# Kernel tuning notes

Measured on AMD Instinct MI355X. Metric: run time of the kernel, lower is better.

## Reference

```python
import jax, jax.numpy as jnp
import numpy as np

H = 12      # heads
P = 4       # dim_point
CHUNK = 256 # chunk_size
DIM_SINGLE = 768
DIM_PAIR = 64
B, N = 1, 1024


def setup_inputs() -> dict:
    key = jax.random.key(0)
    ks = jax.random.split(key, 24)
    s = 0.02
    d = DIM_SINGLE
    inp = {
        'single': jax.random.normal(ks[0], (B, N, d), jnp.float32),
        'pair': jax.random.normal(ks[1], (B, N, N, DIM_PAIR), jnp.float32),
        'rot': jax.random.normal(ks[2], (B, N, 3, 3), jnp.float32),
        'trans': jax.random.normal(ks[3], (B, N, 3), jnp.float32),
        # Linear weights stored as (in, out) so y = x @ W + b
        'Wq': jax.random.normal(ks[4], (d, d), jnp.float32) * s,
        'bq': jnp.zeros((d,), jnp.float32),
        'Wk': jax.random.normal(ks[5], (d, d), jnp.float32) * s,
        'bk': jnp.zeros((d,), jnp.float32),
        'Wv': jax.random.normal(ks[6], (d, d), jnp.float32) * s,
        'bv': jnp.zeros((d,), jnp.float32),
        'Wpb': jax.random.normal(ks[7], (DIM_PAIR, H), jnp.float32) * s,
        'bpb': jnp.zeros((H,), jnp.float32),
        'Wqp': jax.random.normal(ks[8], (d, H * P * 3), jnp.float32) * s,
        'bqp': jnp.zeros((H * P * 3,), jnp.float32),
        'Wkp': jax.random.normal(ks[9], (d, H * P * 3), jnp.float32) * s,
        'bkp': jnp.zeros((H * P * 3,), jnp.float32),
        'Wvp': jax.random.normal(ks[10], (d, H * P * 3), jnp.float32) * s,
        'bvp': jnp.zeros((H * P * 3,), jnp.float32),
        'Wo': jax.random.normal(ks[11], (d, d), jnp.float32) * s,
        'bo': jnp.zeros((d,), jnp.float32),
        'Wpo': jax.random.normal(ks[12], (H * P * 3, d), jnp.float32) * s,
        'bpo': jnp.zeros((d,), jnp.float32),
        'ln_g': jnp.ones((d,), jnp.float32),
        'ln_b': jnp.zeros((d,), jnp.float32),
    }
    return inp


def _layernorm(x, g, b, eps=1e-5):
    mu = jnp.mean(x, axis=-1, keepdims=True)
    var = jnp.mean((x - mu) ** 2, axis=-1, keepdims=True)
    return (x - mu) * jax.lax.rsqrt(var + eps) * g + b


def reference(single, pair, rot, trans, Wq, bq, Wk, bk, Wv, bv, Wpb, bpb,
              Wqp, bqp, Wkp, bkp, Wvp, bvp, Wo, bo, Wpo, bpo, ln_g, ln_b):
    Bs, Ns, C = single.shape
    Ch = C // H
    scale = Ch ** (-0.5)

    q = (single @ Wq + bq).reshape(Bs, Ns, H, Ch)
    k = (single @ Wk + bk).reshape(Bs, Ns, H, Ch)
    v = (single @ Wv + bv).reshape(Bs, Ns, H, Ch)

    # [B,N,N,H] -> [B,H,N,M]
    pair_bias = jnp.transpose(pair @ Wpb + bpb, (0, 3, 1, 2))

    q_pts = (single @ Wqp + bqp).reshape(Bs, Ns, H, P, 3)
    k_pts = (single @ Wkp + bkp).reshape(Bs, Ns, H, P, 3)
    v_pts = (single @ Wvp + bvp).reshape(Bs, Ns, H, P, 3)

    t = trans[:, :, None, None, :]  # [B,N,1,1,3]
    q_pts_g = jnp.einsum('bnhpd,bnde->bnhpe', q_pts, rot) + t
    k_pts_g = jnp.einsum('bnhpd,bnde->bnhpe', k_pts, rot) + t
    v_pts_g = jnp.einsum('bnhpd,bnde->bnhpe', v_pts, rot) + t

    q2_h = jnp.transpose(jnp.sum(q_pts_g ** 2, axis=(3, 4)), (0, 2, 1))  # [B,H,N]
    k2_h = jnp.transpose(jnp.sum(k_pts_g ** 2, axis=(3, 4)), (0, 2, 1))  # [B,H,N]

    scalar_logits = jnp.einsum('bnhc,bmhc->bhnm', q, k) * scale  # [B,H,N,N]

    out_scalar = jnp.zeros((Bs, Ns, H, Ch), single.dtype)
    out_points = jnp.zeros((Bs, Ns, H, P, 3), single.dtype)

    # Faithful to the original: softmax is taken PER CHUNK over the key axis,
    # and the per-chunk weighted sums are accumulated.
    for start in range(0, Ns, CHUNK):
        end = min(start + CHUNK, Ns)
        qk = jnp.einsum('bnhpd,bmhpd->bhnm', q_pts_g, k_pts_g[:, start:end])
        pt_logits = -0.5 * (q2_h[:, :, :, None] + k2_h[:, :, None, start:end]
                            - 2.0 * qk) * scale
        logits = scalar_logits[:, :, :, start:end] + pair_bias[:, :, :, start:end] + pt_logits
        attn = jax.nn.softmax(logits, axis=-1)  # [B,H,N,chunk]
        out_scalar = out_scalar + jnp.einsum('bhnm,bmhc->bnhc', attn, v[:, start:end])
        out_points = out_points + jnp.einsum('bhnm,bmhpd->bnhpd', attn, v_pts_g[:, start:end])

    weighted_scalar = out_scalar.reshape(Bs, Ns, H * Ch)
    weighted_points = out_points.reshape(Bs, Ns, H * P * 3)
    point_proj = weighted_points @ Wpo + bpo
    out = (weighted_scalar + point_proj) @ Wo + bo
    return _layernorm(single + out, ln_g, ln_b)
```

## Files before the change

### kernel.cpp

```cpp
#include <hip/hip_runtime.h>
#include <stdint.h>

#define NTOK 1024
#define NH 12
#define QPSLAB 2801664

typedef short bf16x8 __attribute__((ext_vector_type(8)));
typedef float f32x4 __attribute__((ext_vector_type(4)));
typedef uint32_t u32x4 __attribute__((ext_vector_type(4)));

__device__ __forceinline__ unsigned short f2bf(float f) {
  union { float f; uint32_t u; } x; x.f = f;
  uint32_t r = x.u + 0x7FFFu + ((x.u >> 16) & 1u);
  return (unsigned short)(r >> 16);
}
__device__ __forceinline__ float bf2f(unsigned short u) {
  union { uint32_t u; float f; } x; x.u = ((uint32_t)u) << 16;
  return x.f;
}
__device__ __forceinline__ bf16x8 pack8(float4 a, float4 b) {
  bf16x8 r;
  r[0] = (short)f2bf(a.x); r[1] = (short)f2bf(a.y);
  r[2] = (short)f2bf(a.z); r[3] = (short)f2bf(a.w);
  r[4] = (short)f2bf(b.x); r[5] = (short)f2bf(b.y);
  r[6] = (short)f2bf(b.z); r[7] = (short)f2bf(b.w);
  return r;
}

__global__ __launch_bounds__(256) void prep_k(
    const float* __restrict__ single, const float* __restrict__ Wq,
    const float* __restrict__ Wk, const float* __restrict__ Wv,
    const float* __restrict__ Wqp, const float* __restrict__ Wkp,
    const float* __restrict__ Wvp, const float* __restrict__ Wpo,
    const float* __restrict__ Wo, const float* __restrict__ Wpb,
    const float* __restrict__ bq, const float* __restrict__ bk,
    const float* __restrict__ bv, const float* __restrict__ bqp,
    const float* __restrict__ bkp, const float* __restrict__ bvp,
    unsigned short* __restrict__ sgl, unsigned short* __restrict__ wcat,
    unsigned short* __restrict__ WB, unsigned short* __restrict__ wpoA,
    float* __restrict__ bcat, unsigned short* __restrict__ wpbt)
{
  const int bid = blockIdx.x, t = threadIdx.x;
  if (bid < 2628) {
    __shared__ unsigned short tl[16][72];
    int b = bid;
    const float* src; unsigned short* dst; int N, dstld, rowbase;
    if (b < 1728) {
      int j = b / 576; b -= j * 576;
      src = (j == 0) ? Wq : (j == 1) ? Wk : Wv;
      N = 768; dst = wcat; dstld = 768; rowbase = j * 768;
    } else if (b < 2052) {
      b -= 1728; int j = b / 108; b -= j * 108;
      src = (j == 0) ? Wqp : (j == 1) ? Wkp : Wvp;
      N = 144; dst = wcat; dstld = 768; rowbase = 2304 + j * 144;
    } else {
      b -= 2052; src = Wo; N = 768; dst = WB; dstld = 912; rowbase = 0;
    }
    const int k0 = (b % 12) * 64, n0 = (b / 12) * 16;
#pragma unroll
    for (int i = 0; i < 4; ++i) {
      int kk = (t >> 4) + i * 16;
      int nn = t & 15;
      tl[nn][kk] = f2bf(src[(size_t)(k0 + kk) * N + n0 + nn]);
    }
    __syncthreads();
#pragma unroll
    for (int i = 0; i < 4; ++i) {
      int kk = t & 63;
      int nn = (t >> 6) + i * 4;
      dst[(size_t)(rowbase + n0 + nn) * dstld + k0 + kk] = tl[nn][kk];
    }
    return;
  }
  if (bid < 3396) {
    int i = (bid - 2628) * 256 + t;
    float4 v = *(const float4*)(single + (size_t)i * 4);
    ushort4 o;
    o.x = f2bf(v.x); o.y = f2bf(v.y); o.z = f2bf(v.z); o.w = f2bf(v.w);
    *(ushort4*)(sgl + (size_t)i * 4) = o;
    return;
  }
  if (bid < 3504) {
    int i = (bid - 3396) * 256 + t;
    float4 v = *(const float4*)(Wpo + (size_t)i * 4);
    ushort4 o;
    o.x = f2bf(v.x); o.y = f2bf(v.y); o.z = f2bf(v.z); o.w = f2bf(v.w);
    *(ushort4*)(wpoA + (size_t)i * 4) = o;
    return;
  }
  if (bid < 3515) {
    int idx = (bid - 3504) * 256 + t;
    if (idx < 2736) {
      float v;
      if (idx < 768) v = bq[idx];
      else if (idx < 1536) v = bk[idx - 768];
      else if (idx < 2304) v = bv[idx - 1536];
      else if (idx < 2448) v = bqp[idx - 2304];
      else if (idx < 2592) v = bkp[idx - 2448];
      else v = bvp[idx - 2592];
      bcat[idx] = v;
    }
    return;
  }
  {
    int idx = (bid - 3515) * 256 + t;
    int h = idx >> 6, k = idx & 63;
    wpbt[idx] = (h < 12) ? f2bf(Wpb[k * 12 + h]) : (unsigned short)0;
  }
}

template <int EPI>
__device__ __forceinline__ void gemm_dev(
    unsigned short* As, unsigned short* Bs,
    const unsigned short* __restrict__ A, int lda, int Mact,
    const unsigned short* __restrict__ Bt, int ldb, int Nact,
    int kt0, int ktn, int kmax,
    float* __restrict__ outf, unsigned short* __restrict__ outb, int ldc,
    const float* __restrict__ p0, int mb, int nb, int addbias)
{
  const int t = threadIdx.x;
  const int w = t >> 6, lane = t & 63;
  const int wr = w >> 1, wc = w & 1;
  const int lr = lane & 15, lc = lane >> 4;
  const int m0 = mb * 128, n0 = nb * 128;
  const int r0 = t >> 2, c0 = t & 3;
  const int r1 = r0 + 64;

  f32x4 acc[4][4] = {};
  u32x4 zz = {0u, 0u, 0u, 0u};
  u32x4 pa0, pa1, pq0, pq1;

#define LOAD_AB(KT)                                                              \
  do {                                                                           \
    int k0_ = (KT) * 32;                                                         \
    int g0_ = k0_ + c0 * 8;                                                      \
    pa0 = (g0_ < kmax && (m0 + r0) < Mact)                                       \
              ? *(const u32x4*)(A + (size_t)(m0 + r0) * lda + g0_) : zz;         \
    pa1 = (g0_ < kmax && (m0 + r1) < Mact)                                       \
              ? *(const u32x4*)(A + (size_t)(m0 + r1) * lda + g0_) : zz;         \
    pq0 = (g0_ < kmax && (n0 + r0) < Nact)                                       \
              ? *(const u32x4*)(Bt + (size_t)(n0 + r0) * ldb + g0_) : zz;        \
    pq1 = (g0_ < kmax && (n0 + r1) < Nact)                                       \
              ? *(const u32x4*)(Bt + (size_t)(n0 + r1) * ldb + g0_) : zz;        \
  } while (0)

  LOAD_AB(kt0);
  for (int kt = kt0; kt < kt0 + ktn; ++kt) {
    __syncthreads();
    ((u32x4*)As)[r0 * 4 + c0] = pa0;
    ((u32x4*)As)[r1 * 4 + c0] = pa1;
    ((u32x4*)Bs)[r0 * 4 + c0] = pq0;
    ((u32x4*)Bs)[r1 * 4 + c0] = pq1;
    __syncthreads();
    if (kt + 1 < kt0 + ktn) LOAD_AB(kt + 1);

    bf16x8 af[4], bfr[4];
#pragma unroll
    for (int mi = 0; mi < 4; ++mi) {
      int row = wr * 64 + mi * 16 + lr;
      af[mi] = *(const bf16x8*)(As + (row * 4 + lc) * 8);
    }
#pragma unroll
    for (int ni = 0; ni < 4; ++ni) {
      int row = wc * 64 + ni * 16 + lr;
      bfr[ni] = *(const bf16x8*)(Bs + (row * 4 + lc) * 8);
    }
#pragma unroll
    for (int mi = 0; mi < 4; ++mi)
#pragma unroll
      for (int ni = 0; ni < 4; ++ni)
        acc[mi][ni] = __builtin_amdgcn_mfma_f32_16x16x32_bf16(
            af[mi], bfr[ni], acc[mi][ni], 0, 0, 0);
  }
#undef LOAD_AB

#pragma unroll
  for (int mi = 0; mi < 4; ++mi) {
#pragma unroll
    for (int ni = 0; ni < 4; ++ni) {
#pragma unroll
      for (int r = 0; r < 4; ++r) {
        int row = m0 + wr * 64 + mi * 16 + lc * 4 + r;
        int col = n0 + wc * 64 + ni * 16 + lr;
        if (row < Mact && col < Nact) {
          float v = acc[mi][ni][r];
          if constexpr (EPI == 0) {
            outf[(size_t)row * ldc + col] = addbias ? (v + p0[col]) : v;
          } else {
            outb[(size_t)col * 912 + 768 + row] = f2bf(v);
          }
        }
      }
    }
  }
}

__global__ __launch_bounds__(256) void fat_k(
    const unsigned short* __restrict__ sgl, const unsigned short* __restrict__ wcat,
    const float* __restrict__ bcat, float* __restrict__ qp2,
    const float* __restrict__ pair, const unsigned short* __restrict__ wpbt,
    const float* __restrict__ bpb, unsigned short* __restrict__ pb,
    const unsigned short* __restrict__ wpoA, unsigned short* __restrict__ WB,
    const float* __restrict__ bpo, const float* __restrict__ Wo,
    const float* __restrict__ bo, float* __restrict__ bfused)
{
  __shared__ unsigned short As[128 * 32];
  __shared__ unsigned short Bs[128 * 32];
  const int bid = blockIdx.x;
  const int t = threadIdx.x;

  if (bid < 12) {
    int mb = bid & 1, nb = bid >> 1;
    gemm_dev<1>(As, Bs, wpoA, 768, 144, WB, 912, 768, 0, 24, 768,
                nullptr, WB, 912, nullptr, mb, nb, 0);
    return;
  }
  if (bid < 15) {
    int n = (bid - 12) * 256 + t;
    float s = bo[n];
    for (int j = 0; j < 768; ++j) s += bpo[j] * Wo[(size_t)j * 768 + n];
    bfused[n] = s;
    return;
  }
  if (bid < 367) {
    int pbid = bid - 15;
    int zk = pbid / 176, rem = pbid % 176;
    int mb = rem & 7, nb = rem >> 3;
    gemm_dev<0>(As, Bs, sgl, 768, 1024, wcat, 768, 2736,
                zk * 12, 12, 768,
                qp2 + (size_t)zk * QPSLAB, nullptr, 2736, bcat, mb, nb, zk == 0);
    return;
  }
  {
    const int w = t >> 6, lane = t & 63;
    const int lr = lane & 15, g = lane >> 4;
    bf16x8 wf0 = *(const bf16x8*)(wpbt + lr * 64 + g * 8);
    bf16x8 wf1 = *(const bf16x8*)(wpbt + lr * 64 + 32 + g * 8);
    const float bias_h = (lr < 12) ? bpb[lr] : 0.f;
    const int wid = (bid - 367) * 4 + w;
#pragma unroll
    for (int it = 0; it < 4; ++it) {
      int tile = wid * 4 + it;
      int nm0 = tile * 16;
      const float* src = pair + (size_t)(nm0 + lr) * 64 + g * 8;
      float4 aA = *(const float4*)(src);
      float4 aB = *(const float4*)(src + 4);
      float4 aC = *(const float4*)(src + 32);
      float4 aD = *(const float4*)(src + 36);
      bf16x8 f0 = pack8(aA, aB);
      bf16x8 f1 = pack8(aC, aD);
      f32x4 c = {0.f, 0.f, 0.f, 0.f};
      c = __builtin_amdgcn_mfma_f32_16x16x32_bf16(f0, wf0, c, 0, 0, 0);
      c = __builtin_amdgcn_mfma_f32_16x16x32_bf16(f1, wf1, c, 0, 0, 0);
      if (lr < 12) {
        ushort4 o;
        o.x = f2bf(c[0] + bias_h);
        o.y = f2bf(c[1] + bias_h);
        o.z = f2bf(c[2] + bias_h);
        o.w = f2bf(c[3] + bias_h);
        *(ushort4*)(pb + ((size_t)lr << 20) + (size_t)nm0 + g * 4) = o;
      }
    }
  }
}

__global__ __launch_bounds__(256) void rotate_k(
    const float* __restrict__ qp2, const float* __restrict__ rot,
    const float* __restrict__ trans,
    unsigned short* __restrict__ Acat, unsigned short* __restrict__ Bcat,
    unsigned short* __restrict__ VcatT, float* __restrict__ q2k2)
{
  const int n = blockIdx.x, t = threadIdx.x;
  __shared__ float R[9], T[3], rg[432];
  if (t < 9) R[t] = rot[n * 9 + t];
  if (t >= 9 && t < 12) T[t - 9] = trans[n * 3 + (t - 9)];
  __syncthreads();
  for (int s = t; s < 432; s += 256) {
    int j = s / 144, r = s % 144;
    int h = r / 12, wo = r % 12;
    int e = wo % 3;
    size_t base = (size_t)n * 2736 + 2304 + j * 144 + (r - e);
    float d0 = qp2[base + 0] + qp2[base + 0 + QPSLAB];
    float d1 = qp2[base + 1] + qp2[base + 1 + QPSLAB];
    float d2 = qp2[base + 2] + qp2[base + 2 + QPSLAB];
    float val = d0 * R[e] + d1 * R[3 + e] + d2 * R[6 + e] + T[e];
    rg[s] = val;
    unsigned short bv = f2bf(val);
    if (j == 0)      Acat[((size_t)h * NTOK + n) * 96 + 64 + wo] = bv;
    else if (j == 1) Bcat[((size_t)h * NTOK + n) * 96 + 64 + wo] = bv;
    else             VcatT[((size_t)h * 80 + 64 + wo) * NTOK + n] = bv;
  }
  __syncthreads();
  for (int s = t; s < 2304; s += 256) {
    int j = s / 768, c = s % 768;
    int h = c >> 6, cc = c & 63;
    size_t ix = (size_t)n * 2736 + s;
    unsigned short bv = f2bf(qp2[ix] + qp2[ix + QPSLAB]);
    if (j == 0)      Acat[((size_t)h * NTOK + n) * 96 + cc] = bv;
    else if (j == 1) Bcat[((size_t)h * NTOK + n) * 96 + cc] = bv;
    else             VcatT[((size_t)h * 80 + cc) * NTOK + n] = bv;
  }
  if (t < 240) {
    int h = t / 20, ix = 76 + t % 20;
    Acat[((size_t)h * NTOK + n) * 96 + ix] = 0;
    Bcat[((size_t)h * NTOK + n) * 96 + ix] = 0;
  }
  if (t >= 240 && t < 288) {
    int s = t - 240;
    int h = s / 4, rr = 76 + s % 4;
    VcatT[((size_t)h * 80 + rr) * NTOK + n] = 0;
  }
  if (t < 24) {
    int j = t / 12, h = t % 12;
    float sum = 0.f;
#pragma unroll
    for (int wo = 0; wo < 12; ++wo) {
      float v = rg[j * 144 + h * 12 + wo];
      sum += v * v;
    }
    q2k2[(size_t)(j * NH + h) * NTOK + n] = sum;
  }
}

__global__ __launch_bounds__(256) void attn_k(
    const unsigned short* __restrict__ pb, const unsigned short* __restrict__ Acat,
    const unsigned short* __restrict__ Bcat, const unsigned short* __restrict__ VcatT,
    const float* __restrict__ q2k2, float* __restrict__ acc4)
{
  __shared__ unsigned short Ls[64 * 256];
  __shared__ unsigned short Bs[128 * 104];
  const int t = threadIdx.x, w = t >> 6, lane = t & 63;
  const int lr = lane & 15, lc = lane >> 4;
  const int n0 = blockIdx.x * 64;
  const int m0 = blockIdx.y * 256;
  const int h  = blockIdx.z;

  const unsigned short* Pg = pb + ((size_t)h << 20) + (size_t)n0 * 1024 + m0;
#pragma unroll
  for (int i = 0; i < 8; ++i) {
    int idx = i * 256 + t;
    int row = idx >> 5, sl = idx & 31;
    u32x4 v = *(const u32x4*)(Pg + (size_t)row * 1024 + sl * 8);
    ((u32x4*)Ls)[row * 32 + (sl ^ (row & 7))] = v;
  }
  const unsigned short* Kg = Bcat + ((size_t)h * 1024 + m0) * 96;
#pragma unroll
  for (int i = 0; i < 6; ++i) {
    int idx = i * 256 + t;
    int row = idx / 12, c = idx % 12;
    u32x4 v = *(const u32x4*)(Kg + (size_t)row * 96 + c * 8);
    *(u32x4*)(Bs + row * 104 + c * 8) = v;
  }
  __syncthreads();

  bf16x8 qf[3];
  const unsigned short* Qg = Acat + ((size_t)h * 1024 + n0 + w * 16 + lr) * 96;
#pragma unroll
  for (int kk = 0; kk < 3; ++kk) qf[kk] = *(const bf16x8*)(Qg + kk * 32 + lc * 8);

  f32x4 sa[16];
#pragma unroll
  for (int ct = 0; ct < 16; ++ct) sa[ct] = (f32x4){0.f, 0.f, 0.f, 0.f};

#pragma unroll
  for (int ct = 0; ct < 8; ++ct)
#pragma unroll
    for (int kk = 0; kk < 3; ++kk) {
      bf16x8 kf = *(const bf16x8*)(Bs + (ct * 16 + lr) * 104 + kk * 32 + lc * 8);
      sa[ct] = __builtin_amdgcn_mfma_f32_16x16x32_bf16(kf, qf[kk], sa[ct], 0, 0, 0);
    }
  __syncthreads();
#pragma unroll
  for (int i = 0; i < 6; ++i) {
    int idx = i * 256 + t;
    int row = idx / 12, c = idx % 12;
    u32x4 v = *(const u32x4*)(Kg + (size_t)(128 + row) * 96 + c * 8);
    *(u32x4*)(Bs + row * 104 + c * 8) = v;
  }
  __syncthreads();
#pragma unroll
  for (int ct = 8; ct < 16; ++ct)
#pragma unroll
    for (int kk = 0; kk < 3; ++kk) {
      bf16x8 kf = *(const bf16x8*)(Bs + ((ct - 8) * 16 + lr) * 104 + kk * 32 + lc * 8);
      sa[ct] = __builtin_amdgcn_mfma_f32_16x16x32_bf16(kf, qf[kk], sa[ct], 0, 0, 0);
    }

  const int nrow = w * 16 + lr;
  const float q2v = q2k2[(size_t)h * 1024 + n0 + nrow];
  const float* k2b = q2k2 + 12288 + (size_t)h * 1024 + m0;
  float mx = -1e30f;
#pragma unroll
  for (int ct = 0; ct < 16; ++ct) {
    int sl = (ct * 2 + (lc >> 1)) ^ (nrow & 7);
    const unsigned short* p = Ls + nrow * 256 + sl * 8 + (lc & 1) * 4;
    ushort4 pv = *(const ushort4*)p;
    float4 k2v = *(const float4*)(k2b + ct * 16 + lc * 4);
    sa[ct][0] = 0.125f * sa[ct][0] + bf2f(pv.x) - 0.0625f * (q2v + k2v.x);
    sa[ct][1] = 0.125f * sa[ct][1] + bf2f(pv.y) - 0.0625f * (q2v + k2v.y);
    sa[ct][2] = 0.125f * sa[ct][2] + bf2f(pv.z) - 0.0625f * (q2v + k2v.z);
    sa[ct][3] = 0.125f * sa[ct][3] + bf2f(pv.w) - 0.0625f * (q2v + k2v.w);
    mx = fmaxf(mx, fmaxf(fmaxf(sa[ct][0], sa[ct][1]), fmaxf(sa[ct][2], sa[ct][3])));
  }
  mx = fmaxf(mx, __shfl_xor(mx, 16, 64));
  mx = fmaxf(mx, __shfl_xor(mx, 32, 64));
  float sm = 0.f;
#pragma unroll
  for (int ct = 0; ct < 16; ++ct)
#pragma unroll
    for (int r = 0; r < 4; ++r) { sa[ct][r] = __expf(sa[ct][r] - mx); sm += sa[ct][r]; }
  sm += __shfl_xor(sm, 16, 64);
  sm += __shfl_xor(sm, 32, 64);
  float inv = 1.0f / sm;
#pragma unroll
  for (int ct = 0; ct < 16; ++ct) {
    int sl = (ct * 2 + (lc >> 1)) ^ (nrow & 7);
    unsigned short* p = Ls + nrow * 256 + sl * 8 + (lc & 1) * 4;
    ushort4 pw;
    pw.x = f2bf(sa[ct][0] * inv); pw.y = f2bf(sa[ct][1] * inv);
    pw.z = f2bf(sa[ct][2] * inv); pw.w = f2bf(sa[ct][3] * inv);
    *(ushort4*)p = pw;
  }
  __syncthreads();

  f32x4 acc[5];
#pragma unroll
  for (int nf = 0; nf < 5; ++nf) acc[nf] = (f32x4){0.f, 0.f, 0.f, 0.f};
  const unsigned short* Vg = VcatT + (size_t)h * 80 * NTOK + m0;
#pragma unroll
  for (int kk = 0; kk < 8; ++kk) {
    int row = w * 16 + lr;
    int sl = (kk * 4 + lc) ^ (row & 7);
    bf16x8 a = *(const bf16x8*)(Ls + row * 256 + sl * 8);
#pragma unroll
    for (int nf = 0; nf < 5; ++nf) {
      int c = nf * 16 + lr;
      bf16x8 b = *(const bf16x8*)(Vg + (size_t)c * NTOK + kk * 32 + lc * 8);
      acc[nf] = __builtin_amdgcn_mfma_f32_16x16x32_bf16(a, b, acc[nf], 0, 0, 0);
    }
  }
  float* out = acc4 + ((size_t)blockIdx.y * NH + h) * (size_t)NTOK * 80;
#pragma unroll
  for (int nf = 0; nf < 5; ++nf)
#pragma unroll
    for (int r = 0; r < 4; ++r) {
      int orow = n0 + w * 16 + lc * 4 + r;
      int c = nf * 16 + lr;
      out[(size_t)orow * 80 + c] = acc[nf][r];
    }
}

__global__ __launch_bounds__(256) void reduce_k(
    const float* __restrict__ acc4, unsigned short* __restrict__ AW)
{
  int idx = blockIdx.x * 256 + threadIdx.x;
  int n = idx / 912, c = idx % 912;
  const size_t cs = (size_t)NH * NTOK * 80;
  size_t base;
  if (c < 768) {
    int h = c >> 6, cc = c & 63;
    base = ((size_t)h * NTOK + n) * 80 + cc;
  } else {
    int c2 = c - 768;
    int h = c2 / 12, wo = c2 % 12;
    base = ((size_t)h * NTOK + n) * 80 + 64 + wo;
  }
  float v = acc4[base] + acc4[base + cs] + acc4[base + 2 * cs] + acc4[base + 3 * cs];
  AW[(size_t)n * 912 + c] = f2bf(v);
}

__global__ __launch_bounds__(256) void tail_gemm_k(
    const unsigned short* __restrict__ AW, const unsigned short* __restrict__ WB,
    float* __restrict__ outpre)
{
  __shared__ unsigned short As[128 * 32];
  __shared__ unsigned short Bs[128 * 32];
  int z = blockIdx.z;
  int kt0 = z * 8, ktn = (z < 3) ? 8 : 5;
  gemm_dev<0>(As, Bs, AW, 912, 1024, WB, 912, 768, kt0, ktn, 912,
              outpre + (size_t)z * 786432, nullptr, 768, nullptr,
              blockIdx.x, blockIdx.y, 0);
}

__global__ __launch_bounds__(256) void ln_k(
    const float* __restrict__ single, const float* __restrict__ outpre,
    const float* __restrict__ bfused, const float* __restrict__ g,
    const float* __restrict__ b, float* __restrict__ out)
{
  const int row = blockIdx.x, t = threadIdx.x;
  __shared__ float red[8];
  size_t base = (size_t)row * 768;
  const size_t SL = 786432;
  float x0 = single[base + t] + bfused[t]
           + outpre[base + t] + outpre[base + t + SL]
           + outpre[base + t + 2 * SL] + outpre[base + t + 3 * SL];
  float x1 = single[base + t + 256] + bfused[t + 256]
           + outpre[base + t + 256] + outpre[base + t + 256 + SL]
           + outpre[base + t + 256 + 2 * SL] + outpre[base + t + 256 + 3 * SL];
  float x2 = single[base + t + 512] + bfused[t + 512]
           + outpre[base + t + 512] + outpre[base + t + 512 + SL]
           + outpre[base + t + 512 + 2 * SL] + outpre[base + t + 512 + 3 * SL];
  float s = x0 + x1 + x2;
#pragma unroll
  for (int off = 32; off; off >>= 1) s += __shfl_xor(s, off, 64);
  if ((t & 63) == 0) red[t >> 6] = s;
  __syncthreads();
  float mu = (red[0] + red[1] + red[2] + red[3]) * (1.0f / 768.0f);
  float d0 = x0 - mu, d1 = x1 - mu, d2 = x2 - mu;
  float vs = d0 * d0 + d1 * d1 + d2 * d2;
#pragma unroll
  for (int off = 32; off; off >>= 1) vs += __shfl_xor(vs, off, 64);
  if ((t & 63) == 0) red[4 + (t >> 6)] = vs;
  __syncthreads();
  float var = (red[4] + red[5] + red[6] + red[7]) * (1.0f / 768.0f);
  float rs = rsqrtf(var + 1e-5f);
  out[base + t]       = d0 * rs * g[t]       + b[t];
  out[base + t + 256] = d1 * rs * g[t + 256] + b[t + 256];
  out[base + t + 512] = d2 * rs * g[t + 512] + b[t + 512];
}

extern "C" void kernel_launch(void* const* d_in, const int* in_sizes, int n_in,
                              void* d_out, int out_size, void* d_ws, size_t ws_size,
                              hipStream_t stream)
{
  (void)in_sizes; (void)n_in; (void)out_size; (void)ws_size;
  const float* single = (const float*)d_in[0];
  const float* pair   = (const float*)d_in[1];
  const float* rot    = (const float*)d_in[2];
  const float* trans  = (const float*)d_in[3];
  const float* Wq  = (const float*)d_in[4];  const float* bq  = (const float*)d_in[5];
  const float* Wk  = (const float*)d_in[6];  const float* bk  = (const float*)d_in[7];
  const float* Wv  = (const float*)d_in[8];  const float* bv  = (const float*)d_in[9];
  const float* Wpb = (const float*)d_in[10]; const float* bpb = (const float*)d_in[11];
  const float* Wqp = (const float*)d_in[12]; const float* bqp = (const float*)d_in[13];
  const float* Wkp = (const float*)d_in[14]; const float* bkp = (const float*)d_in[15];
  const float* Wvp = (const float*)d_in[16]; const float* bvp = (const float*)d_in[17];
  const float* Wo  = (const float*)d_in[18]; const float* bo  = (const float*)d_in[19];
  const float* Wpo = (const float*)d_in[20]; const float* bpo = (const float*)d_in[21];
  const float* lng = (const float*)d_in[22]; const float* lnb = (const float*)d_in[23];

  char* ws = (char*)d_ws;
  unsigned short* sgl    = (unsigned short*)(ws + 0);
  unsigned short* wcat   = (unsigned short*)(ws + 1572864);
  unsigned short* wpoA   = (unsigned short*)(ws + 5775360);
  unsigned short* WB     = (unsigned short*)(ws + 5996544);
  float*          bcat   = (float*)(ws + 7397376);
  unsigned short* wpbt   = (unsigned short*)(ws + 7408384);
  float*          bfused = (float*)(ws + 7410432);
  float*          qp2    = (float*)(ws + 7413504);
  unsigned short* Acat   = (unsigned short*)(ws + 29826816);
  unsigned short* Bcat   = (unsigned short*)(ws + 32186112);
  unsigned short* VcatT  = (unsigned short*)(ws + 34545408);
  float*          q2k2   = (float*)(ws + 36511488);
  unsigned short* pb     = (unsigned short*)(ws + 36609792);
  float*          acc4   = (float*)(ws + 61775616);
  unsigned short* AW     = (unsigned short*)(ws + 77504256);
  float*          outpre = (float*)(ws + 79372032);

  prep_k<<<3519, 256, 0, stream>>>(single, Wq, Wk, Wv, Wqp, Wkp, Wvp, Wpo, Wo,
                                   Wpb, bq, bk, bv, bqp, bkp, bvp,
                                   sgl, wcat, WB, wpoA, bcat, wpbt);

  fat_k<<<4463, 256, 0, stream>>>(sgl, wcat, bcat, qp2, pair, wpbt, bpb, pb,
                                  wpoA, WB, bpo, Wo, bo, bfused);

  rotate_k<<<1024, 256, 0, stream>>>(qp2, rot, trans, Acat, Bcat, VcatT, q2k2);

  attn_k<<<dim3(16, 4, 12), 256, 0, stream>>>(pb, Acat, Bcat, VcatT, q2k2, acc4);

  reduce_k<<<3648, 256, 0, stream>>>(acc4, AW);

  tail_gemm_k<<<dim3(8, 6, 4), 256, 0, stream>>>(AW, WB, outpre);

  ln_k<<<1024, 256, 0, stream>>>(single, outpre, bfused, lng, lnb, (float*)d_out);
}
```

Measured before the change: 159.8 us.

## Use packed bf16 conversion intrinsics, prefetch pair loads, reorder fat kernel blocks

Replaces the manual float-to-bf16 rounding with packed __float22bfloat162_rn conversions in pack8, the pair-bias store and the softmax store. The pair-bias blocks now come first in the fat kernel and software-prefetch the next tile's pair rows, with the GEMM blocks moved to the end of the grid. It also adds a bounds guard in reduce_k, tidies the layernorm loads, and shifts the wpbt workspace offset. The intent is to cut conversion ALU work and hide pair load latency; the block reordering changes how the tail of the grid overlaps.

```diff
diff --git a/kernel.cpp b/kernel.cpp
--- a/kernel.cpp
+++ b/kernel.cpp
@@ -1,4 +1,5 @@
 #include <hip/hip_runtime.h>
+#include <hip/hip_bf16.h>
 #include <stdint.h>
 
 #define NTOK 1024
@@ -19,12 +20,12 @@
   return x.f;
 }
 __device__ __forceinline__ bf16x8 pack8(float4 a, float4 b) {
-  bf16x8 r;
-  r[0] = (short)f2bf(a.x); r[1] = (short)f2bf(a.y);
-  r[2] = (short)f2bf(a.z); r[3] = (short)f2bf(a.w);
-  r[4] = (short)f2bf(b.x); r[5] = (short)f2bf(b.y);
-  r[6] = (short)f2bf(b.z); r[7] = (short)f2bf(b.w);
-  return r;
+  union { __hip_bfloat162 h2[4]; bf16x8 v; } u;
+  u.h2[0] = __float22bfloat162_rn(make_float2(a.x, a.y));
+  u.h2[1] = __float22bfloat162_rn(make_float2(a.z, a.w));
+  u.h2[2] = __float22bfloat162_rn(make_float2(b.x, b.y));
+  u.h2[3] = __float22bfloat162_rn(make_float2(b.z, b.w));
+  return u.v;
 }
 
 __global__ __launch_bounds__(256) void prep_k(
@@ -204,63 +205,70 @@
     const float* __restrict__ bpo, const float* __restrict__ Wo,
     const float* __restrict__ bo, float* __restrict__ bfused)
 {
-  __shared__ unsigned short As[128 * 32];
-  __shared__ unsigned short Bs[128 * 32];
   const int bid = blockIdx.x;
   const int t = threadIdx.x;
 
-  if (bid < 12) {
-    int mb = bid & 1, nb = bid >> 1;
-    gemm_dev<1>(As, Bs, wpoA, 768, 144, WB, 912, 768, 0, 24, 768,
-                nullptr, WB, 912, nullptr, mb, nb, 0);
-    return;
-  }
-  if (bid < 15) {
-    int n = (bid - 12) * 256 + t;
-    float s = bo[n];
-    for (int j = 0; j < 768; ++j) s += bpo[j] * Wo[(size_t)j * 768 + n];
-    bfused[n] = s;
-    return;
-  }
-  if (bid < 367) {
-    int pbid = bid - 15;
-    int zk = pbid / 176, rem = pbid % 176;
-    int mb = rem & 7, nb = rem >> 3;
-    gemm_dev<0>(As, Bs, sgl, 768, 1024, wcat, 768, 2736,
-                zk * 12, 12, 768,
-                qp2 + (size_t)zk * QPSLAB, nullptr, 2736, bcat, mb, nb, zk == 0);
-    return;
-  }
-  {
+  if (bid < 4096) {
     const int w = t >> 6, lane = t & 63;
     const int lr = lane & 15, g = lane >> 4;
     bf16x8 wf0 = *(const bf16x8*)(wpbt + lr * 64 + g * 8);
     bf16x8 wf1 = *(const bf16x8*)(wpbt + lr * 64 + 32 + g * 8);
     const float bias_h = (lr < 12) ? bpb[lr] : 0.f;
-    const int wid = (bid - 367) * 4 + w;
+    const int wid = bid * 4 + w;
+    const float* s = pair + ((size_t)(wid * 64) + lr) * 64 + g * 8;
+    float4 nA = *(const float4*)(s);
+    float4 nB = *(const float4*)(s + 4);
+    float4 nC = *(const float4*)(s + 32);
+    float4 nD = *(const float4*)(s + 36);
 #pragma unroll
     for (int it = 0; it < 4; ++it) {
-      int tile = wid * 4 + it;
-      int nm0 = tile * 16;
-      const float* src = pair + (size_t)(nm0 + lr) * 64 + g * 8;
-      float4 aA = *(const float4*)(src);
-      float4 aB = *(const float4*)(src + 4);
-      float4 aC = *(const float4*)(src + 32);
-      float4 aD = *(const float4*)(src + 36);
+      float4 aA = nA, aB = nB, aC = nC, aD = nD;
+      if (it < 3) {
+        const float* p = s + (size_t)(it + 1) * 1024;
+        nA = *(const float4*)(p);
+        nB = *(const float4*)(p + 4);
+        nC = *(const float4*)(p + 32);
+        nD = *(const float4*)(p + 36);
+      }
       bf16x8 f0 = pack8(aA, aB);
       bf16x8 f1 = pack8(aC, aD);
       f32x4 c = {0.f, 0.f, 0.f, 0.f};
       c = __builtin_amdgcn_mfma_f32_16x16x32_bf16(f0, wf0, c, 0, 0, 0);
       c = __builtin_amdgcn_mfma_f32_16x16x32_bf16(f1, wf1, c, 0, 0, 0);
       if (lr < 12) {
-        ushort4 o;
-        o.x = f2bf(c[0] + bias_h);
-        o.y = f2bf(c[1] + bias_h);
-        o.z = f2bf(c[2] + bias_h);
-        o.w = f2bf(c[3] + bias_h);
-        *(ushort4*)(pb + ((size_t)lr << 20) + (size_t)nm0 + g * 4) = o;
+        int nm0 = (wid * 4 + it) * 16;
+        union { __hip_bfloat162 h2[2]; ushort4 s4; } pu;
+        pu.h2[0] = __float22bfloat162_rn(make_float2(c[0] + bias_h, c[1] + bias_h));
+        pu.h2[1] = __float22bfloat162_rn(make_float2(c[2] + bias_h, c[3] + bias_h));
+        *(ushort4*)(pb + ((size_t)lr << 20) + (size_t)nm0 + g * 4) = pu.s4;
       }
     }
+    return;
+  }
+
+  __shared__ unsigned short As[128 * 32];
+  __shared__ unsigned short Bs[128 * 32];
+  int rb = bid - 4096;
+  if (rb < 12) {
+    int mb = rb & 1, nb = rb >> 1;
+    gemm_dev<1>(As, Bs, wpoA, 768, 144, WB, 912, 768, 0, 24, 768,
+                nullptr, WB, 912, nullptr, mb, nb, 0);
+    return;
+  }
+  if (rb < 15) {
+    int n = (rb - 12) * 256 + t;
+    float sacc = bo[n];
+    for (int j = 0; j < 768; ++j) sacc += bpo[j] * Wo[(size_t)j * 768 + n];
+    bfused[n] = sacc;
+    return;
+  }
+  {
+    int pbid = rb - 15;
+    int zk = pbid / 176, rem = pbid % 176;
+    int mb = rem & 7, nb = rem >> 3;
+    gemm_dev<0>(As, Bs, sgl, 768, 1024, wcat, 768, 2736,
+                zk * 12, 12, 768,
+                qp2 + (size_t)zk * QPSLAB, nullptr, 2736, bcat, mb, nb, zk == 0);
   }
 }
 
@@ -416,10 +424,10 @@
   for (int ct = 0; ct < 16; ++ct) {
     int sl = (ct * 2 + (lc >> 1)) ^ (nrow & 7);
     unsigned short* p = Ls + nrow * 256 + sl * 8 + (lc & 1) * 4;
-    ushort4 pw;
-    pw.x = f2bf(sa[ct][0] * inv); pw.y = f2bf(sa[ct][1] * inv);
-    pw.z = f2bf(sa[ct][2] * inv); pw.w = f2bf(sa[ct][3] * inv);
-    *(ushort4*)p = pw;
+    union { __hip_bfloat162 h2[2]; ushort4 s4; } pu;
+    pu.h2[0] = __float22bfloat162_rn(make_float2(sa[ct][0] * inv, sa[ct][1] * inv));
+    pu.h2[1] = __float22bfloat162_rn(make_float2(sa[ct][2] * inv, sa[ct][3] * inv));
+    *(ushort4*)p = pu.s4;
   }
   __syncthreads();
 
@@ -454,6 +462,7 @@
     const float* __restrict__ acc4, unsigned short* __restrict__ AW)
 {
   int idx = blockIdx.x * 256 + threadIdx.x;
+  if (idx >= 1024 * 912) return;
   int n = idx / 912, c = idx % 912;
   const size_t cs = (size_t)NH * NTOK * 80;
   size_t base;
@@ -491,22 +500,22 @@
   __shared__ float red[8];
   size_t base = (size_t)row * 768;
   const size_t SL = 786432;
-  float x0 = single[base + t] + bfused[t]
-           + outpre[base + t] + outpre[base + t + SL]
-           + outpre[base + t + 2 * SL] + outpre[base + t + 3 * SL];
-  float x1 = single[base + t + 256] + bfused[t + 256]
-           + outpre[base + t + 256] + outpre[base + t + 256 + SL]
-           + outpre[base + t + 256 + 2 * SL] + outpre[base + t + 256 + 3 * SL];
-  float x2 = single[base + t + 512] + bfused[t + 512]
-           + outpre[base + t + 512] + outpre[base + t + 512 + SL]
-           + outpre[base + t + 512 + 2 * SL] + outpre[base + t + 512 + 3 * SL];
-  float s = x0 + x1 + x2;
+  float x[3];
+#pragma unroll
+  for (int j = 0; j < 3; ++j) {
+    int c = t + j * 256;
+    float v = single[base + c] + bfused[c];
+#pragma unroll
+    for (int z = 0; z < 4; ++z) v += outpre[base + c + (size_t)z * SL];
+    x[j] = v;
+  }
+  float s = x[0] + x[1] + x[2];
 #pragma unroll
   for (int off = 32; off; off >>= 1) s += __shfl_xor(s, off, 64);
   if ((t & 63) == 0) red[t >> 6] = s;
   __syncthreads();
   float mu = (red[0] + red[1] + red[2] + red[3]) * (1.0f / 768.0f);
-  float d0 = x0 - mu, d1 = x1 - mu, d2 = x2 - mu;
+  float d0 = x[0] - mu, d1 = x[1] - mu, d2 = x[2] - mu;
   float vs = d0 * d0 + d1 * d1 + d2 * d2;
 #pragma unroll
   for (int off = 32; off; off >>= 1) vs += __shfl_xor(vs, off, 64);
@@ -545,7 +554,7 @@
   unsigned short* wpoA   = (unsigned short*)(ws + 5775360);
   unsigned short* WB     = (unsigned short*)(ws + 5996544);
   float*          bcat   = (float*)(ws + 7397376);
-  unsigned short* wpbt   = (unsigned short*)(ws + 7408384);
+  unsigned short* wpbt   = (unsigned short*)(ws + 7408320);
   float*          bfused = (float*)(ws + 7410432);
   float*          qp2    = (float*)(ws + 7413504);
   unsigned short* Acat   = (unsigned short*)(ws + 29826816);
```

Measured after the change: 192.1 us. 20.2% more time.
